# Kernel optimization log

Hardware: AMD Instinct MI355X
Metric: run time of the kernel (lower is better)

The kernel has to match this reference:

```python
import jax, jax.numpy as jnp
import numpy as np
import math

NEG = -1000000.0


def setup_inputs() -> dict:
    key = jax.random.key(0)
    ks = jax.random.split(key, 8)
    B, S, D = 4, 2048, 1024
    std = 1.0 / math.sqrt(D)
    return {
        "queries": jax.random.normal(ks[0], (B, S, D), jnp.float32),
        "keys": jax.random.normal(ks[1], (B, S, D), jnp.float32),
        "values": jax.random.normal(ks[2], (B, S, D), jnp.float32),
        "valid_len": jax.random.randint(ks[3], (B,), 1, S, dtype=jnp.int64 if jax.config.jax_enable_x64 else jnp.int32),
        "W_q": jax.random.normal(ks[4], (D, D), jnp.float32) * std,
        "W_k": jax.random.normal(ks[5], (D, D), jnp.float32) * std,
        "W_v": jax.random.normal(ks[6], (D, D), jnp.float32) * std,
        "W_o": jax.random.normal(ks[7], (D, D), jnp.float32) * std,
    }


def reference(queries, keys, values, valid_len, W_q, W_k, W_v, W_o):
    NUM_HEADS = 16
    B, S, D = queries.shape
    hd = D // NUM_HEADS

    def split_heads(x):
        # (B, S, D) -> (B, H, S, hd)
        return x.reshape(B, -1, NUM_HEADS, hd).transpose(0, 2, 1, 3)

    # nn.Linear with weight W applies x @ W.T
    q = split_heads(queries @ W_q.T)
    k = split_heads(keys @ W_k.T)
    v = split_heads(values @ W_v.T)

    scale = 1.0 / math.sqrt(hd)
    scores = jnp.einsum('bhqd,bhkd->bhqk', q, k) * scale  # (B, H, Sq, Sk)

    # key-padding mask from valid_len: positions >= valid_len are masked
    kpos = jnp.arange(scores.shape[-1])
    pad_mask = kpos[None, None, None, :] >= valid_len[:, None, None, None]
    scores = jnp.where(pad_mask, NEG, scores)
    attn = jax.nn.softmax(scores, axis=-1)

    out = jnp.einsum('bhqk,bhkd->bhqd', attn, v)  # (B, H, Sq, hd)
    out = out.transpose(0, 2, 1, 3).reshape(B, -1, D)
    return out @ W_o.T
```

## Files before the change

### kernel.cpp

```cpp
#include <hip/hip_runtime.h>
#include <hip/hip_bf16.h>

using bf16_t = __bf16;
using bf16x8 = __attribute__((ext_vector_type(8))) __bf16;
using bf16x4 = __attribute__((ext_vector_type(4))) __bf16;
using f32x4  = __attribute__((ext_vector_type(4))) float;

#define S_  2048
#define D_  1024

typedef __attribute__((address_space(1))) unsigned int glb_u32;
typedef __attribute__((address_space(3))) unsigned int lds_u32;

__device__ __forceinline__ void async_cp16(const void* g, void* lds) {
    __builtin_amdgcn_global_load_lds(
        (glb_u32*)(unsigned long long)g,
        (lds_u32*)(unsigned int)(unsigned long long)lds,
        16, 0, 0);
}

__global__ __launch_bounds__(256) void cast4_f32_bf16(const float* __restrict__ a, const float* __restrict__ b,
                                                      const float* __restrict__ c, const float* __restrict__ dd,
                                                      bf16_t* __restrict__ oa, bf16_t* __restrict__ ob,
                                                      bf16_t* __restrict__ oc, bf16_t* __restrict__ od, int n4) {
    int i = blockIdx.x * 256 + threadIdx.x;
    if (i >= n4) return;
    const float* s; bf16_t* d;
    int w = blockIdx.y;
    if      (w == 0) { s = a;  d = oa; }
    else if (w == 1) { s = b;  d = ob; }
    else if (w == 2) { s = c;  d = oc; }
    else             { s = dd; d = od; }
    float4 f = reinterpret_cast<const float4*>(s)[i];
    bf16x4 o;
    o[0] = (bf16_t)f.x; o[1] = (bf16_t)f.y; o[2] = (bf16_t)f.z; o[3] = (bf16_t)f.w;
    reinterpret_cast<bf16x4*>(d)[i] = o;
}

__global__ __launch_bounds__(256) void qkv_gemm(const float* __restrict__ qf,
                                                const float* __restrict__ kf,
                                                const float* __restrict__ vf,
                                                const bf16_t* __restrict__ Wqb,
                                                const bf16_t* __restrict__ Wkb,
                                                const bf16_t* __restrict__ Wvb,
                                                bf16_t* __restrict__ Qp,
                                                bf16_t* __restrict__ Kp,
                                                bf16_t* __restrict__ Vt,
                                                float cs) {
    __shared__ bf16_t As[2][128 * 32];
    __shared__ bf16_t Bs[2][128 * 32];
    const int K = 1024;
    int tid  = threadIdx.x;
    int lane = tid & 63;
    int w    = tid >> 6;
    int l15  = lane & 15, quad = lane >> 4;

    int bid = blockIdx.x;
    int xcd = bid & 7, idx = bid >> 3;
    int z   = idx >> 6;
    int rem = idx & 63;
    int m0 = (xcd * 8 + (rem & 7)) * 128;
    int n0 = (rem >> 3) * 128;
    int wm = (w >> 1) * 64, wn = (w & 1) * 64;

    const float*  Af; const bf16_t* Bt;
    if      (z == 0) { Af = qf; Bt = Wqb; }
    else if (z == 1) { Af = kf; Bt = Wkb; }
    else             { Af = vf; Bt = Wvb; }
    float scale = (z == 0) ? cs : 1.0f;

    const float* Ag = Af + (size_t)(m0 + (tid >> 2)) * K + (tid & 3) * 8;

    int arow = tid >> 2, aslot = tid & 3;
    int aoff = arow * 32 + ((aslot ^ ((arow >> 1) & 3)) * 8);

    const bf16_t* bSrc[2]; bf16_t* bDst0[2], *bDst1[2];
#pragma unroll
    for (int j = 0; j < 2; j++) {
        int linear = j * 256 + tid;
        int row = linear >> 2, s = linear & 3;
        bSrc[j]  = Bt + (size_t)(n0 + row) * K + ((s ^ ((row >> 1) & 3)) * 8);
        bDst0[j] = &Bs[0][linear * 8];
        bDst1[j] = &Bs[1][linear * 8];
    }

    float4 a0, a1, a2, a3;
    auto loadA = [&](int k0) {
        const float* p = Ag + k0;
        a0 = *reinterpret_cast<const float4*>(p);
        a1 = *reinterpret_cast<const float4*>(p + 4);
        a2 = *reinterpret_cast<const float4*>(p + (size_t)64 * K);
        a3 = *reinterpret_cast<const float4*>(p + (size_t)64 * K + 4);
    };
    auto storeA = [&](bf16_t* dst) {
        bf16x8 o0, o1;
        o0[0] = (bf16_t)a0.x; o0[1] = (bf16_t)a0.y; o0[2] = (bf16_t)a0.z; o0[3] = (bf16_t)a0.w;
        o0[4] = (bf16_t)a1.x; o0[5] = (bf16_t)a1.y; o0[6] = (bf16_t)a1.z; o0[7] = (bf16_t)a1.w;
        o1[0] = (bf16_t)a2.x; o1[1] = (bf16_t)a2.y; o1[2] = (bf16_t)a2.z; o1[3] = (bf16_t)a2.w;
        o1[4] = (bf16_t)a3.x; o1[5] = (bf16_t)a3.y; o1[6] = (bf16_t)a3.z; o1[7] = (bf16_t)a3.w;
        *reinterpret_cast<bf16x8*>(dst + aoff)        = o0;
        *reinterpret_cast<bf16x8*>(dst + aoff + 2048) = o1;
    };

    f32x4 acc[4][4] = {};

    loadA(0);
    async_cp16(bSrc[0], bDst0[0]);
    async_cp16(bSrc[1], bDst0[1]);
    storeA(As[0]);
    __syncthreads();

    for (int k0 = 0; k0 < K; k0 += 32) {
        int cur = (k0 >> 5) & 1;
        bool more = (k0 + 32 < K);
        if (more) {
            int nxt = cur ^ 1;
            loadA(k0 + 32);
            async_cp16(bSrc[0] + k0 + 32, nxt ? bDst1[0] : bDst0[0]);
            async_cp16(bSrc[1] + k0 + 32, nxt ? bDst1[1] : bDst0[1]);
        }
        bf16x8 af[4], bfr[4];
#pragma unroll
        for (int t = 0; t < 4; t++) {
            int ra = wm + t * 16 + l15;
            int rb = wn + t * 16 + l15;
            af[t]  = *reinterpret_cast<const bf16x8*>(&As[cur][ra * 32 + ((quad ^ ((ra >> 1) & 3)) * 8)]);
            bfr[t] = *reinterpret_cast<const bf16x8*>(&Bs[cur][rb * 32 + ((quad ^ ((rb >> 1) & 3)) * 8)]);
        }
#pragma unroll
        for (int mt = 0; mt < 4; mt++)
#pragma unroll
            for (int nt = 0; nt < 4; nt++)
                acc[mt][nt] = __builtin_amdgcn_mfma_f32_16x16x32_bf16(af[mt], bfr[nt], acc[mt][nt], 0, 0, 0);
        if (more) storeA(As[cur ^ 1]);
        __syncthreads();
    }

    if (z == 2) {
#pragma unroll
        for (int mt = 0; mt < 4; mt++)
#pragma unroll
            for (int nt = 0; nt < 4; nt++) {
                int m = m0 + wm + mt * 16 + quad * 4;
                int n = n0 + wn + nt * 16 + l15;
                bf16x4 o4;
#pragma unroll
                for (int r = 0; r < 4; r++) o4[r] = (bf16_t)acc[mt][nt][r];
                size_t vrow = (size_t)((m >> 11) * 16 + (n >> 6)) * 64 + (n & 63);
                int ml = m & 2047;
                int mp = (ml & ~31) | (((ml >> 2) & 3) << 3) | (((ml >> 4) & 1) << 2);
                *reinterpret_cast<bf16x4*>(&Vt[vrow * S_ + mp]) = o4;
            }
    } else {
        bf16_t* Co = (z == 0) ? Qp : Kp;
#pragma unroll
        for (int mt = 0; mt < 4; mt++)
#pragma unroll
            for (int nt = 0; nt < 4; nt++)
#pragma unroll
                for (int r = 0; r < 4; r++) {
                    int m = m0 + wm + mt * 16 + quad * 4 + r;
                    int n = n0 + wn + nt * 16 + l15;
                    Co[(size_t)m * 1024 + n] = (bf16_t)(acc[mt][nt][r] * scale);
                }
    }
}

__global__ __launch_bounds__(256) void gemm_out(const bf16_t* __restrict__ A,
                                                const bf16_t* __restrict__ Bt,
                                                float* __restrict__ C) {
    __shared__ bf16_t As[3][128 * 32];
    __shared__ bf16_t Bs[3][128 * 32];
    const int K = 1024;
    int tid  = threadIdx.x;
    int lane = tid & 63;
    int w    = tid >> 6;
    int l15  = lane & 15, quad = lane >> 4;

    int bid = blockIdx.x;
    int xcd = bid & 7, idx = bid >> 3;
    int m0 = (xcd * 8 + (idx & 7)) * 128;
    int n0 = (idx >> 3) * 128;
    int wm = (w >> 1) * 64, wn = (w & 1) * 64;

    const bf16_t* aSrc[2]; const bf16_t* bSrc[2];
    int dOff[2];
#pragma unroll
    for (int j = 0; j < 2; j++) {
        int linear = j * 256 + tid;
        int row = linear >> 2, s = linear & 3;
        int sw = (s ^ ((row >> 1) & 3)) * 8;
        aSrc[j] = A  + (size_t)(m0 + row) * K + sw;
        bSrc[j] = Bt + (size_t)(n0 + row) * K + sw;
        dOff[j] = linear * 8;
    }

    auto stage = [&](int buf, int koff) {
#pragma unroll
        for (int j = 0; j < 2; j++) async_cp16(aSrc[j] + koff, &As[buf][dOff[j]]);
#pragma unroll
        for (int j = 0; j < 2; j++) async_cp16(bSrc[j] + koff, &Bs[buf][dOff[j]]);
    };

    f32x4 acc[4][4] = {};

    stage(0, 0);
    stage(1, 32);

    int cur = 0, nx2 = 2;
    for (int i = 0; i < 32; ++i) {
        if (i == 31) asm volatile("s_waitcnt vmcnt(0)" ::: "memory");
        else         asm volatile("s_waitcnt vmcnt(4)" ::: "memory");
        __builtin_amdgcn_s_barrier();
        if (i + 2 < 32) stage(nx2, (i + 2) * 32);

        bf16x8 af[4], bfr[4];
#pragma unroll
        for (int t = 0; t < 4; t++) {
            int ra = wm + t * 16 + l15;
            int rb = wn + t * 16 + l15;
            af[t]  = *reinterpret_cast<const bf16x8*>(&As[cur][ra * 32 + ((quad ^ ((ra >> 1) & 3)) * 8)]);
            bfr[t] = *reinterpret_cast<const bf16x8*>(&Bs[cur][rb * 32 + ((quad ^ ((rb >> 1) & 3)) * 8)]);
        }
#pragma unroll
        for (int mt = 0; mt < 4; mt++)
#pragma unroll
            for (int nt = 0; nt < 4; nt++)
                acc[mt][nt] = __builtin_amdgcn_mfma_f32_16x16x32_bf16(af[mt], bfr[nt], acc[mt][nt], 0, 0, 0);

        cur = (cur == 2) ? 0 : cur + 1;
        nx2 = (nx2 == 2) ? 0 : nx2 + 1;
    }

#pragma unroll
    for (int mt = 0; mt < 4; mt++)
#pragma unroll
        for (int nt = 0; nt < 4; nt++)
#pragma unroll
            for (int r = 0; r < 4; r++) {
                int m = m0 + wm + mt * 16 + quad * 4 + r;
                int n = n0 + wn + nt * 16 + l15;
                C[(size_t)m * 1024 + n] = acc[mt][nt][r];
            }
}

__global__ __launch_bounds__(256) void attn_fused(const bf16_t* __restrict__ Qp,
                                                  const bf16_t* __restrict__ Kp,
                                                  const bf16_t* __restrict__ Vt,
                                                  const int* __restrict__ vlen_p,
                                                  bf16_t* __restrict__ Out) {
    __shared__ bf16_t smem[6][64 * 64];

    int tid  = threadIdx.x;
    int lane = tid & 63, w = tid >> 6;
    int l15  = lane & 15, quad = lane >> 4;

    int nk[4], ord[4] = {0, 1, 2, 3};
#pragma unroll
    for (int i = 0; i < 4; i++) nk[i] = (vlen_p[i] + 63) >> 6;
#pragma unroll
    for (int i = 0; i < 3; i++)
#pragma unroll
        for (int j = 0; j < 3 - i; j++)
            if (nk[ord[j + 1]] > nk[ord[j]]) { int t = ord[j]; ord[j] = ord[j + 1]; ord[j + 1] = t; }

    int bid  = blockIdx.x;
    int b    = ord[bid >> 9];
    int t    = bid & 511;
    int h    = (t & 7) * 2 + ((t >> 3) & 1);
    int qblk = t >> 4;
    int vlen = vlen_p[b];
    int nkb  = (vlen + 63) >> 6;

    const bf16_t* Kg = Kp + (size_t)b * S_ * D_ + h * 64;
    const bf16_t* Vg = Vt + (size_t)(b * 16 + h) * 64 * S_;

    bf16x8 qf[2];
    {
        int qrow = w * 16 + l15;
        const bf16_t* qp = Qp + (size_t)(b * S_ + qblk * 64 + qrow) * D_ + h * 64 + quad * 8;
        qf[0] = *reinterpret_cast<const bf16x8*>(qp);
        qf[1] = *reinterpret_cast<const bf16x8*>(qp + 32);
    }

    int r0 = tid >> 3, s0 = tid & 7;
    int sx = (s0 ^ (r0 & 7)) * 8;
    const bf16_t* kB = Kg + (size_t)r0 * D_ + sx;
    const bf16_t* vB = Vg + (size_t)r0 * S_ + sx;

    auto stage = [&](int slot, int tile) {
        const bf16_t* kp = kB + (size_t)tile * 64 * D_;
        const bf16_t* vp = vB + tile * 64;
        async_cp16(kp,                    smem[slot]     + tid * 8);
        async_cp16(kp + (size_t)32 * D_,  smem[slot]     + tid * 8 + 2048);
        async_cp16(vp,                    smem[3 + slot] + tid * 8);
        async_cp16(vp + (size_t)32 * S_,  smem[3 + slot] + tid * 8 + 2048);
    };

    stage(0, 0);
    stage(1, nkb > 1 ? 1 : 0);

    f32x4 o[4] = {};
    float l_st = 0.f;

    int cur = 0, nx2 = 2;
    for (int kb = 0; kb < nkb; kb++) {
        asm volatile("s_waitcnt vmcnt(4)" ::: "memory");
        __builtin_amdgcn_s_barrier();
        {
            int tnext = kb + 2 < nkb ? kb + 2 : nkb - 1;
            stage(nx2, tnext);
        }
        const bf16_t* Kc = smem[cur];
        const bf16_t* Vc = smem[3 + cur];

        f32x4 sc[4] = {};
#pragma unroll
        for (int nt = 0; nt < 4; nt++) {
            int row = nt * 16 + l15, x = row & 7;
#pragma unroll
            for (int kk = 0; kk < 2; kk++) {
                bf16x8 kf = *reinterpret_cast<const bf16x8*>(&Kc[row * 64 + ((kk * 4 + quad) ^ x) * 8]);
                sc[nt] = __builtin_amdgcn_mfma_f32_16x16x32_bf16(kf, qf[kk], sc[nt], 0, 0, 0);
            }
        }

        bool partial = (vlen & 63) && (kb == nkb - 1);
        bf16x8 pf[2];
        float lacc = 0.f;
        if (!partial) {
#pragma unroll
            for (int nt = 0; nt < 4; nt++)
#pragma unroll
                for (int r = 0; r < 4; r++) {
                    float p = __builtin_exp2f(sc[nt][r]);
                    lacc += p;
                    pf[nt >> 1][(nt & 1) * 4 + r] = (bf16_t)p;
                }
        } else {
#pragma unroll
            for (int nt = 0; nt < 4; nt++)
#pragma unroll
                for (int r = 0; r < 4; r++) {
                    float p = __builtin_exp2f(sc[nt][r]);
                    if (kb * 64 + nt * 16 + quad * 4 + r >= vlen) p = 0.f;
                    lacc += p;
                    pf[nt >> 1][(nt & 1) * 4 + r] = (bf16_t)p;
                }
        }
        l_st += lacc;

#pragma unroll
        for (int np = 0; np < 2; np++)
#pragma unroll
            for (int dt = 0; dt < 4; dt++) {
                int row = dt * 16 + l15, x = row & 7;
                bf16x8 vfr = *reinterpret_cast<const bf16x8*>(&Vc[row * 64 + ((np * 4 + quad) ^ x) * 8]);
                o[dt] = __builtin_amdgcn_mfma_f32_16x16x32_bf16(vfr, pf[np], o[dt], 0, 0, 0);
            }

        cur = (cur == 2) ? 0 : cur + 1;
        nx2 = (nx2 == 2) ? 0 : nx2 + 1;
    }

    float l = l_st;
    l += __shfl_xor(l, 16);
    l += __shfl_xor(l, 32);
    float inv = 1.0f / l;

    __syncthreads();
    bf16_t* T = smem[0];
    {
        int row = w * 16 + l15, x = row & 7;
#pragma unroll
        for (int dt = 0; dt < 4; dt++) {
            bf16x4 o4;
#pragma unroll
            for (int r = 0; r < 4; r++) o4[r] = (bf16_t)(o[dt][r] * inv);
            int slot = dt * 2 + (quad >> 1);
            *reinterpret_cast<bf16x4*>(&T[row * 64 + (slot ^ x) * 8 + (quad & 1) * 4]) = o4;
        }
    }
    __syncthreads();
    {
        int row = tid >> 2, ch = tid & 3, x = row & 7;
        size_t obase = (size_t)(b * S_ + qblk * 64 + row) * D_ + h * 64 + ch * 16;
        bf16x8 f0 = *reinterpret_cast<const bf16x8*>(&T[row * 64 + ((ch * 2)     ^ x) * 8]);
        bf16x8 f1 = *reinterpret_cast<const bf16x8*>(&T[row * 64 + ((ch * 2 + 1) ^ x) * 8]);
        *reinterpret_cast<bf16x8*>(&Out[obase])     = f0;
        *reinterpret_cast<bf16x8*>(&Out[obase + 8]) = f1;
    }
}

extern "C" void kernel_launch(void* const* d_in, const int* in_sizes, int n_in,
                              void* d_out, int out_size, void* d_ws, size_t ws_size,
                              hipStream_t stream) {
    const float* q  = (const float*)d_in[0];
    const float* k  = (const float*)d_in[1];
    const float* v  = (const float*)d_in[2];
    const int*   vl = (const int*)d_in[3];
    const float* Wq = (const float*)d_in[4];
    const float* Wk = (const float*)d_in[5];
    const float* Wv = (const float*)d_in[6];
    const float* Wo = (const float*)d_in[7];
    float* out = (float*)d_out;

    bf16_t* ws = (bf16_t*)d_ws;
    const size_t SD = (size_t)8192 * 1024;
    const size_t WW = (size_t)1024 * 1024;
    bf16_t* tmpB = ws + SD;
    bf16_t* Qp   = ws + 2 * SD;
    bf16_t* Kp   = ws + 3 * SD;
    bf16_t* Vt   = ws + 4 * SD;
    bf16_t* Wqb  = ws + 5 * SD;
    bf16_t* Wkb  = Wqb + WW;
    bf16_t* Wvb  = Wqb + 2 * WW;
    bf16_t* Wob  = Wqb + 3 * WW;

    const float cs = 0.18033688f;
    dim3 blk(256);

    cast4_f32_bf16<<<dim3(1024, 4), blk, 0, stream>>>(Wq, Wk, Wv, Wo, Wqb, Wkb, Wvb, Wob, 262144);
    qkv_gemm<<<dim3(1536), blk, 0, stream>>>(q, k, v, Wqb, Wkb, Wvb, Qp, Kp, Vt, cs);
    attn_fused<<<dim3(2048), blk, 0, stream>>>(Qp, Kp, Vt, vl, tmpB);
    gemm_out<<<dim3(512), blk, 0, stream>>>(tmpB, Wob, out);
}
```

Before: 331.4 us.

## Deepen QKV GEMM prefetch and switch attention to two-stage LDS pipeline

The QKV projection GEMM now triple-buffers the weight tiles in LDS. It keeps two register sets of fp32 activation loads in flight, prefetching two k-steps ahead. It waits with explicit vmcnt instead of a full __syncthreads and requests 4 blocks per CU through launch bounds. The attention kernel drops from a three-slot to a two-slot K/V ring, which cuts LDS from 48KB to 32KB to allow more resident blocks. It also stages Q through LDS with async copies and ends each iteration with a full barrier. This trades prefetch depth in attention for occupancy, and adds register pressure to the GEMM.

```diff
diff --git a/kernel.cpp b/kernel.cpp
--- a/kernel.cpp
+++ b/kernel.cpp
@@ -37,18 +37,18 @@
     reinterpret_cast<bf16x4*>(d)[i] = o;
 }
 
-__global__ __launch_bounds__(256) void qkv_gemm(const float* __restrict__ qf,
-                                                const float* __restrict__ kf,
-                                                const float* __restrict__ vf,
-                                                const bf16_t* __restrict__ Wqb,
-                                                const bf16_t* __restrict__ Wkb,
-                                                const bf16_t* __restrict__ Wvb,
-                                                bf16_t* __restrict__ Qp,
-                                                bf16_t* __restrict__ Kp,
-                                                bf16_t* __restrict__ Vt,
-                                                float cs) {
+__global__ __launch_bounds__(256, 4) void qkv_gemm(const float* __restrict__ qf,
+                                                   const float* __restrict__ kf,
+                                                   const float* __restrict__ vf,
+                                                   const bf16_t* __restrict__ Wqb,
+                                                   const bf16_t* __restrict__ Wkb,
+                                                   const bf16_t* __restrict__ Wvb,
+                                                   bf16_t* __restrict__ Qp,
+                                                   bf16_t* __restrict__ Kp,
+                                                   bf16_t* __restrict__ Vt,
+                                                   float cs) {
     __shared__ bf16_t As[2][128 * 32];
-    __shared__ bf16_t Bs[2][128 * 32];
+    __shared__ bf16_t Bs[3][128 * 32];
     const int K = 1024;
     int tid  = threadIdx.x;
     int lane = tid & 63;
@@ -74,66 +74,75 @@
     int arow = tid >> 2, aslot = tid & 3;
     int aoff = arow * 32 + ((aslot ^ ((arow >> 1) & 3)) * 8);
 
-    const bf16_t* bSrc[2]; bf16_t* bDst0[2], *bDst1[2];
+    const bf16_t* bSrc[2]; int bOff[2];
 #pragma unroll
     for (int j = 0; j < 2; j++) {
         int linear = j * 256 + tid;
         int row = linear >> 2, s = linear & 3;
-        bSrc[j]  = Bt + (size_t)(n0 + row) * K + ((s ^ ((row >> 1) & 3)) * 8);
-        bDst0[j] = &Bs[0][linear * 8];
-        bDst1[j] = &Bs[1][linear * 8];
-    }
-
-    float4 a0, a1, a2, a3;
-    auto loadA = [&](int k0) {
+        bSrc[j] = Bt + (size_t)(n0 + row) * K + ((s ^ ((row >> 1) & 3)) * 8);
+        bOff[j] = linear * 8;
+    }
+
+    float4 aE[4], aO[4];
+    auto loadA = [&](float4* a, int k0) {
         const float* p = Ag + k0;
-        a0 = *reinterpret_cast<const float4*>(p);
-        a1 = *reinterpret_cast<const float4*>(p + 4);
-        a2 = *reinterpret_cast<const float4*>(p + (size_t)64 * K);
-        a3 = *reinterpret_cast<const float4*>(p + (size_t)64 * K + 4);
+        a[0] = *reinterpret_cast<const float4*>(p);
+        a[1] = *reinterpret_cast<const float4*>(p + 4);
+        a[2] = *reinterpret_cast<const float4*>(p + (size_t)64 * K);
+        a[3] = *reinterpret_cast<const float4*>(p + (size_t)64 * K + 4);
     };
-    auto storeA = [&](bf16_t* dst) {
+    auto storeA = [&](bf16_t* dst, const float4* a) {
         bf16x8 o0, o1;
-        o0[0] = (bf16_t)a0.x; o0[1] = (bf16_t)a0.y; o0[2] = (bf16_t)a0.z; o0[3] = (bf16_t)a0.w;
-        o0[4] = (bf16_t)a1.x; o0[5] = (bf16_t)a1.y; o0[6] = (bf16_t)a1.z; o0[7] = (bf16_t)a1.w;
-        o1[0] = (bf16_t)a2.x; o1[1] = (bf16_t)a2.y; o1[2] = (bf16_t)a2.z; o1[3] = (bf16_t)a2.w;
-        o1[4] = (bf16_t)a3.x; o1[5] = (bf16_t)a3.y; o1[6] = (bf16_t)a3.z; o1[7] = (bf16_t)a3.w;
+        o0[0] = (bf16_t)a[0].x; o0[1] = (bf16_t)a[0].y; o0[2] = (bf16_t)a[0].z; o0[3] = (bf16_t)a[0].w;
+        o0[4] = (bf16_t)a[1].x; o0[5] = (bf16_t)a[1].y; o0[6] = (bf16_t)a[1].z; o0[7] = (bf16_t)a[1].w;
+        o1[0] = (bf16_t)a[2].x; o1[1] = (bf16_t)a[2].y; o1[2] = (bf16_t)a[2].z; o1[3] = (bf16_t)a[2].w;
+        o1[4] = (bf16_t)a[3].x; o1[5] = (bf16_t)a[3].y; o1[6] = (bf16_t)a[3].z; o1[7] = (bf16_t)a[3].w;
         *reinterpret_cast<bf16x8*>(dst + aoff)        = o0;
         *reinterpret_cast<bf16x8*>(dst + aoff + 2048) = o1;
     };
+    auto stageB = [&](bf16_t* dst, int k0) {
+        async_cp16(bSrc[0] + k0, dst + bOff[0]);
+        async_cp16(bSrc[1] + k0, dst + bOff[1]);
+    };
 
     f32x4 acc[4][4] = {};
-
-    loadA(0);
-    async_cp16(bSrc[0], bDst0[0]);
-    async_cp16(bSrc[1], bDst0[1]);
-    storeA(As[0]);
-    __syncthreads();
-
-    for (int k0 = 0; k0 < K; k0 += 32) {
-        int cur = (k0 >> 5) & 1;
-        bool more = (k0 + 32 < K);
-        if (more) {
-            int nxt = cur ^ 1;
-            loadA(k0 + 32);
-            async_cp16(bSrc[0] + k0 + 32, nxt ? bDst1[0] : bDst0[0]);
-            async_cp16(bSrc[1] + k0 + 32, nxt ? bDst1[1] : bDst0[1]);
-        }
+    bf16_t *bRead = Bs[0], *bMid = Bs[1], *bStage = Bs[2];
+
+    loadA(aE, 0);
+    stageB(Bs[0], 0);
+    loadA(aO, 32);
+    stageB(Bs[1], 32);
+    storeA(As[0], aE);
+    asm volatile("s_waitcnt vmcnt(6) lgkmcnt(0)" ::: "memory");
+    __builtin_amdgcn_s_barrier();
+
+#pragma unroll 2
+    for (int i = 0; i < 32; ++i) {
+        int k2 = (i + 2 < 32) ? (i + 2) * 32 : 992;
+        float4* aNew = (i & 1) ? aO : aE;
+        loadA(aNew, k2);
+        stageB(bStage, k2);
+
+        const bf16_t* Ac = As[i & 1];
         bf16x8 af[4], bfr[4];
 #pragma unroll
         for (int t = 0; t < 4; t++) {
             int ra = wm + t * 16 + l15;
             int rb = wn + t * 16 + l15;
-            af[t]  = *reinterpret_cast<const bf16x8*>(&As[cur][ra * 32 + ((quad ^ ((ra >> 1) & 3)) * 8)]);
-            bfr[t] = *reinterpret_cast<const bf16x8*>(&Bs[cur][rb * 32 + ((quad ^ ((rb >> 1) & 3)) * 8)]);
+            af[t]  = *reinterpret_cast<const bf16x8*>(&Ac[ra * 32 + ((quad ^ ((ra >> 1) & 3)) * 8)]);
+            bfr[t] = *reinterpret_cast<const bf16x8*>(&bRead[rb * 32 + ((quad ^ ((rb >> 1) & 3)) * 8)]);
         }
 #pragma unroll
         for (int mt = 0; mt < 4; mt++)
 #pragma unroll
             for (int nt = 0; nt < 4; nt++)
                 acc[mt][nt] = __builtin_amdgcn_mfma_f32_16x16x32_bf16(af[mt], bfr[nt], acc[mt][nt], 0, 0, 0);
-        if (more) storeA(As[cur ^ 1]);
-        __syncthreads();
+
+        if (i + 1 < 32) storeA(As[(i + 1) & 1], (i & 1) ? aE : aO);
+
+        bf16_t* t0 = bRead; bRead = bMid; bMid = bStage; bStage = t0;
+        asm volatile("s_waitcnt vmcnt(6) lgkmcnt(0)" ::: "memory");
+        __builtin_amdgcn_s_barrier();
     }
 
     if (z == 2) {
@@ -249,7 +258,7 @@
                                                   const bf16_t* __restrict__ Vt,
                                                   const int* __restrict__ vlen_p,
                                                   bf16_t* __restrict__ Out) {
-    __shared__ bf16_t smem[6][64 * 64];
+    __shared__ bf16_t smem[4][64 * 64];
 
     int tid  = threadIdx.x;
     int lane = tid & 63, w = tid >> 6;
@@ -272,47 +281,53 @@
     int vlen = vlen_p[b];
     int nkb  = (vlen + 63) >> 6;
 
+    const bf16_t* Qg = Qp + (size_t)(b * S_ + qblk * 64) * D_ + h * 64;
     const bf16_t* Kg = Kp + (size_t)b * S_ * D_ + h * 64;
     const bf16_t* Vg = Vt + (size_t)(b * 16 + h) * 64 * S_;
 
+    int r0 = tid >> 3, s0 = tid & 7;
+    int sx = (s0 ^ (r0 & 7)) * 8;
+    const bf16_t* kS0 = Kg + (size_t)r0 * D_ + sx;
+    const bf16_t* kS1 = kS0 + (size_t)32 * D_;
+    const bf16_t* vS0 = Vg + (size_t)r0 * S_ + sx;
+    const bf16_t* vS1 = vS0 + (size_t)32 * S_;
+
+    {
+        const bf16_t* qS0 = Qg + (size_t)r0 * D_ + sx;
+        async_cp16(qS0,                   smem[2] + tid * 8);
+        async_cp16(qS0 + (size_t)32 * D_, smem[2] + tid * 8 + 2048);
+        async_cp16(kS0, smem[0] + tid * 8);
+        async_cp16(kS1, smem[0] + tid * 8 + 2048);
+        async_cp16(vS0, smem[1] + tid * 8);
+        async_cp16(vS1, smem[1] + tid * 8 + 2048);
+    }
+    __syncthreads();
+
     bf16x8 qf[2];
     {
-        int qrow = w * 16 + l15;
-        const bf16_t* qp = Qp + (size_t)(b * S_ + qblk * 64 + qrow) * D_ + h * 64 + quad * 8;
-        qf[0] = *reinterpret_cast<const bf16x8*>(qp);
-        qf[1] = *reinterpret_cast<const bf16x8*>(qp + 32);
-    }
-
-    int r0 = tid >> 3, s0 = tid & 7;
-    int sx = (s0 ^ (r0 & 7)) * 8;
-    const bf16_t* kB = Kg + (size_t)r0 * D_ + sx;
-    const bf16_t* vB = Vg + (size_t)r0 * S_ + sx;
-
-    auto stage = [&](int slot, int tile) {
-        const bf16_t* kp = kB + (size_t)tile * 64 * D_;
-        const bf16_t* vp = vB + tile * 64;
-        async_cp16(kp,                    smem[slot]     + tid * 8);
-        async_cp16(kp + (size_t)32 * D_,  smem[slot]     + tid * 8 + 2048);
-        async_cp16(vp,                    smem[3 + slot] + tid * 8);
-        async_cp16(vp + (size_t)32 * S_,  smem[3 + slot] + tid * 8 + 2048);
-    };
-
-    stage(0, 0);
-    stage(1, nkb > 1 ? 1 : 0);
+        int row = w * 16 + l15, x = row & 7;
+#pragma unroll
+        for (int kk = 0; kk < 2; kk++)
+            qf[kk] = *reinterpret_cast<const bf16x8*>(&smem[2][row * 64 + ((kk * 4 + quad) ^ x) * 8]);
+    }
+    __syncthreads();
 
     f32x4 o[4] = {};
     float l_st = 0.f;
 
-    int cur = 0, nx2 = 2;
     for (int kb = 0; kb < nkb; kb++) {
-        asm volatile("s_waitcnt vmcnt(4)" ::: "memory");
-        __builtin_amdgcn_s_barrier();
-        {
-            int tnext = kb + 2 < nkb ? kb + 2 : nkb - 1;
-            stage(nx2, tnext);
-        }
-        const bf16_t* Kc = smem[cur];
-        const bf16_t* Vc = smem[3 + cur];
+        int cur = kb & 1;
+        if (kb + 1 < nkb) {
+            int nxt = cur ^ 1;
+            kS0 += (size_t)64 * D_; kS1 += (size_t)64 * D_;
+            vS0 += 64;              vS1 += 64;
+            async_cp16(kS0, smem[nxt * 2]     + tid * 8);
+            async_cp16(kS1, smem[nxt * 2]     + tid * 8 + 2048);
+            async_cp16(vS0, smem[nxt * 2 + 1] + tid * 8);
+            async_cp16(vS1, smem[nxt * 2 + 1] + tid * 8 + 2048);
+        }
+        const bf16_t* Kc = smem[cur * 2];
+        const bf16_t* Vc = smem[cur * 2 + 1];
 
         f32x4 sc[4] = {};
 #pragma unroll
@@ -359,8 +374,7 @@
                 o[dt] = __builtin_amdgcn_mfma_f32_16x16x32_bf16(vfr, pf[np], o[dt], 0, 0, 0);
             }
 
-        cur = (cur == 2) ? 0 : cur + 1;
-        nx2 = (nx2 == 2) ? 0 : nx2 + 1;
+        __syncthreads();
     }
 
     float l = l_st;
@@ -368,7 +382,6 @@
     l += __shfl_xor(l, 32);
     float inv = 1.0f / l;
 
-    __syncthreads();
     bf16_t* T = smem[0];
     {
         int row = w * 16 + l15, x = row & 7;
```

Measured after the change: 311.9 us. -5.9%, faster.
